# Kernel tuning notes

Hardware: AMD Instinct MI355X
Metric: run time of the kernel (lower is better)

Reference implementation:

```python
import jax, jax.numpy as jnp
import numpy as np
import math

E = 768      # embed_dim
N = 16       # ssm state_dim
K = 4        # d_conv
R = 48       # dt_rank = ceil(E/16)
DEPTH = 4
V = 32000    # vocab
B = 2
L = 1024
T = 100
H = 4 * E    # mlp hidden


def layer_norm(x, g, b):
    mu = jnp.mean(x, axis=-1, keepdims=True)
    var = jnp.mean(jnp.square(x - mu), axis=-1, keepdims=True)
    return (x - mu) * jax.lax.rsqrt(var + 1e-5) * g + b


def sin_emb(t, dim):
    half = dim // 2
    freqs = jnp.exp(-math.log(10000.0) * jnp.arange(half, dtype=jnp.float32) / half)
    args = t.astype(jnp.float32)[:, None] * freqs
    return jnp.concatenate([jnp.sin(args), jnp.cos(args)], axis=-1)


def ssm_forward(x, z_w, p_w, conv_w, dtp_w, dtp_b, A_log, Dp, out_w):
    # x: (B, L, E)
    z = x @ z_w.T
    params = x @ p_w.T                      # (B, L, R+2N)
    dt_un, _B_unused, Cp = jnp.split(params, [R, R + N], axis=-1)
    dt = jax.nn.softplus(dt_un @ dtp_w.T + dtp_b)   # (B, L, E)
    # depthwise causal conv (torch pads both sides d_conv-1 then trims -> left pad only)
    xc = jax.lax.conv_general_dilated(
        jnp.transpose(x, (0, 2, 1)), conv_w, (1,), [(K - 1, 0)],
        feature_group_count=E, dimension_numbers=('NCH', 'OIH', 'NCH'))
    u = jax.nn.silu(jnp.transpose(xc, (0, 2, 1)))   # (B, L, E)
    A = -jnp.exp(A_log)                              # (E, N)
    A_t = jnp.exp(dt[..., None] * A)                 # (B, L, E, N)
    B_t = jnp.where(jnp.abs(A) < 1e-5, dt[..., None], (A_t - 1.0) / (A + 1e-10))
    # recurrence exactly as source: h[0]=B[0]*u[0]; h[t]=A[t-1]*h[t-1]+B[t-1]*u[t-1]
    h0 = B_t[:, 0] * u[:, 0, :, None]                # (B, E, N)
    xs = (jnp.moveaxis(A_t[:, :-1], 1, 0),
          jnp.moveaxis(B_t[:, :-1], 1, 0),
          jnp.moveaxis(u[:, :-1], 1, 0))
    def step(h, inp):
        a, b, uu = inp
        h = a * h + b * uu[..., None]
        return h, h
    _, hs = jax.lax.scan(step, h0, xs)               # (L-1, B, E, N)
    h_all = jnp.concatenate([h0[None], hs], axis=0)  # (L, B, E, N)
    y = jnp.einsum('bln,lben->ble', Cp, h_all)
    y = y + u * Dp
    return (y * jax.nn.silu(z)) @ out_w.T


def setup_inputs() -> dict:
    key = jax.random.key(0)
    ks = list(jax.random.split(key, 32))
    it = iter(ks)
    def nrm(shape, fan_in):
        return jax.random.normal(next(it), shape, jnp.float32) * np.sqrt(2.0 / fan_in)
    d = {}
    d['tokens'] = jax.random.randint(next(it), (B, L), 0, V + 1)
    d['timesteps'] = jax.random.randint(next(it), (B,), 0, T)
    d['tok_emb'] = jax.random.normal(next(it), (V + 1, E), jnp.float32) * 0.02
    d['time_w1'] = nrm((H, E), E); d['time_b1'] = jnp.zeros((H,), jnp.float32)
    d['time_w2'] = nrm((E, H), H); d['time_b2'] = jnp.zeros((E,), jnp.float32)
    d['ln1_g'] = jnp.ones((DEPTH, E), jnp.float32); d['ln1_b'] = jnp.zeros((DEPTH, E), jnp.float32)
    d['z_w'] = nrm((DEPTH, E, E), E)
    d['p_w'] = nrm((DEPTH, R + 2 * N, E), E)
    d['conv_w'] = jax.random.normal(next(it), (DEPTH, E, 1, K), jnp.float32) * np.sqrt(1.0 / K)
    s = R ** -0.5 * 0.1
    d['dtp_w'] = jax.random.uniform(next(it), (DEPTH, E, R), jnp.float32, -s, s)
    d['dtp_b'] = jnp.full((DEPTH, E), math.log(math.expm1(0.001)), jnp.float32)
    d['A_log'] = jnp.tile(jnp.log(jnp.arange(1, N + 1, dtype=jnp.float32)), (DEPTH, E, 1))
    d['D_param'] = jnp.ones((DEPTH, E), jnp.float32)
    d['out_w'] = nrm((DEPTH, E, E), E)
    d['ln2_g'] = jnp.ones((DEPTH, E), jnp.float32); d['ln2_b'] = jnp.zeros((DEPTH, E), jnp.float32)
    d['mlp_w1'] = nrm((DEPTH, H, E), E); d['mlp_b1'] = jnp.zeros((DEPTH, H), jnp.float32)
    d['mlp_w2'] = nrm((DEPTH, E, H), H); d['mlp_b2'] = jnp.zeros((DEPTH, E), jnp.float32)
    d['lnout_g'] = jnp.ones((E,), jnp.float32); d['lnout_b'] = jnp.zeros((E,), jnp.float32)
    d['head_w'] = nrm((V, E), E); d['head_b'] = jnp.zeros((V,), jnp.float32)
    return d


def reference(tokens, timesteps, tok_emb, time_w1, time_b1, time_w2, time_b2,
              ln1_g, ln1_b, z_w, p_w, conv_w, dtp_w, dtp_b, A_log, D_param, out_w,
              ln2_g, ln2_b, mlp_w1, mlp_b1, mlp_w2, mlp_b2,
              lnout_g, lnout_b, head_w, head_b):
    temb = sin_emb(timesteps, E)
    temb = jax.nn.silu(temb @ time_w1.T + time_b1) @ time_w2.T + time_b2
    x = tok_emb[tokens] + temb[:, None, :]           # (B, L, E)
    for i in range(DEPTH):
        x = x + ssm_forward(layer_norm(x, ln1_g[i], ln1_b[i]),
                            z_w[i], p_w[i], conv_w[i], dtp_w[i], dtp_b[i],
                            A_log[i], D_param[i], out_w[i])
        h = layer_norm(x, ln2_g[i], ln2_b[i])
        h = jax.nn.gelu(h @ mlp_w1[i].T + mlp_b1[i], approximate=False) @ mlp_w2[i].T + mlp_b2[i]
        x = x + h
    x = layer_norm(x, lnout_g, lnout_b)
    return x @ head_w.T + head_b                     # (B, L, V)
```

## Files before the change

kernel.cpp:

```cpp
#include <hip/hip_runtime.h>
#include <math.h>

#define EE 768
#define NS 16
#define RR 48
#define NDEPTH 4
#define NB 2
#define NL 1024
#define NH 3072
#define NV 32000
#define M_ROWS (NB*NL)
#define NC 64
#define CL 16
#define ZPW 896
#define LOG2E 1.44269504088896f
#define LN2   0.69314718055995f

typedef __attribute__((ext_vector_type(8))) __bf16 bf16x8;
typedef __attribute__((ext_vector_type(4))) __bf16 bf16x4;
typedef __attribute__((ext_vector_type(4))) float f32x4;

__device__ __forceinline__ void gl_lds16(const __bf16* g, __bf16* l){
  __builtin_amdgcn_global_load_lds(
      (const __attribute__((address_space(1))) void*)g,
      (__attribute__((address_space(3))) void*)l, 16, 0, 0);
}

enum { BE_STORE=0, BE_BIAS=1, BE_RESID=2, BE_BIAS_RESID=3, BE_BIAS_GELU_B16=4,
       BE_STORE_ZP=5 };

template<int EPI, int BMT, int BNT>
__global__ __launch_bounds__(256) void gemm_bf16(const __bf16* __restrict__ A,
    const __bf16* __restrict__ W, const float* __restrict__ bias,
    void* __restrict__ Cv, float* __restrict__ dtf, int N, int K, int gx, int gy)
{
  const int nwg = gx*gy;
  const int orig = blockIdx.x;
  const int q = nwg >> 3, r = nwg & 7;
  const int xcd = orig & 7, bse = orig >> 3;
  int wg = (xcd < r ? xcd*(q+1) : r*(q+1) + (xcd-r)*q) + bse;
  const int GN = 16;
  const int per = gy*GN;
  const int g = wg / per;
  const int gstart = g*GN;
  const int gw0 = gx - gstart;
  const int gw = (GN < gw0) ? GN : gw0;
  const int local = wg - g*per;
  const int bx = gstart + local % gw;
  const int by = local / gw;

  constexpr int MFR = BMT/32;
  constexpr int NFR = BNT/32;
  __shared__ __bf16 As[BMT][64];
  __shared__ __bf16 Ws[BNT][64];
  const int bm = by*BMT, bn = bx*BNT;
  const int tid = threadIdx.x;
  const int w = tid>>6, lane = tid&63;
  const int wr = w>>1, wc = w&1;
  const int fr = lane&15, kg = lane>>4;
  const int sr8 = lane>>3;
  const int sg  = lane&7;
  const int ksrc = ((sg ^ sr8) & 7)*8;

  f32x4 acc[MFR][NFR];
  #pragma unroll
  for (int m=0;m<MFR;m++)
    #pragma unroll
    for (int n=0;n<NFR;n++)
      acc[m][n] = (f32x4){0.f,0.f,0.f,0.f};

  for (int k0=0;k0<K;k0+=64){
    const __bf16* gA = A + (size_t)(bm + w*(BMT/4) + sr8)*K + k0 + ksrc;
    #pragma unroll
    for (int c8=0;c8<BMT/32;c8++)
      gl_lds16(gA + (size_t)(c8*8)*K, &As[w*(BMT/4) + c8*8][0]);
    const __bf16* gW = W + (size_t)(bn + w*(BNT/4) + sr8)*K + k0 + ksrc;
    #pragma unroll
    for (int c8=0;c8<BNT/32;c8++)
      gl_lds16(gW + (size_t)(c8*8)*K, &Ws[w*(BNT/4) + c8*8][0]);
    __syncthreads();
    #pragma unroll
    for (int kk=0;kk<2;kk++){
      const int sp = (((kg + kk*4) ^ (fr&7)) & 7) * 8;
      bf16x8 af[MFR], bfr[NFR];
      #pragma unroll
      for (int m=0;m<MFR;m++) af[m]  = *(const bf16x8*)&As[wr*(BMT/2) + m*16 + fr][sp];
      #pragma unroll
      for (int n=0;n<NFR;n++) bfr[n] = *(const bf16x8*)&Ws[wc*(BNT/2) + n*16 + fr][sp];
      #pragma unroll
      for (int m=0;m<MFR;m++)
        #pragma unroll
        for (int n=0;n<NFR;n++)
          acc[m][n] = __builtin_amdgcn_mfma_f32_16x16x32_bf16(af[m], bfr[n], acc[m][n], 0,0,0);
    }
    __syncthreads();
  }

  float* Cf = (float*)Cv;
  __bf16* Cb = (__bf16*)Cv;
  #pragma unroll
  for (int m=0;m<MFR;m++){
    int row = bm + wr*(BMT/2) + m*16 + kg*4;
    #pragma unroll
    for (int n=0;n<NFR;n++){
      int col = bn + wc*(BNT/2) + n*16 + fr;
      float bsv = 0.f;
      if (EPI==BE_BIAS || EPI==BE_BIAS_RESID || EPI==BE_BIAS_GELU_B16)
        bsv = bias[col];
      #pragma unroll
      for (int rr2=0;rr2<4;rr2++){
        float v = acc[m][n][rr2];
        size_t idx = (size_t)(row+rr2)*N + col;
        if (EPI==BE_STORE)            Cf[idx] = v;
        else if (EPI==BE_BIAS)        Cf[idx] = v + bsv;
        else if (EPI==BE_RESID)       Cf[idx] += v;
        else if (EPI==BE_BIAS_RESID)  Cf[idx] += v + bsv;
        else if (EPI==BE_BIAS_GELU_B16){
          float xg = v + bsv; Cb[idx] = (__bf16)(0.5f*xg*(1.f+erff(xg*0.70710678118654752f)));
        } else if (EPI==BE_STORE_ZP){
          Cf[idx] = v;
          if (col >= 768 && col < 816) dtf[(size_t)(row+rr2)*RR + (col-768)] = v;
        }
      }
    }
  }
}

#define S1E 2752512LL
#define S2E 5111808LL
#define S3E 14548992LL
#define S4E 23986176LL
#define STOT 48562176LL

__global__ void f2b_all(const float* __restrict__ zw, const float* __restrict__ pw,
                        const float* __restrict__ ow, const float* __restrict__ m1,
                        const float* __restrict__ m2, const float* __restrict__ hw,
                        __bf16* __restrict__ o){
  long long idx = ((long long)blockIdx.x*256 + threadIdx.x)*4;
  if (idx >= STOT) return;
  float4 v;
  if (idx < S1E){
    long long layer = idx / (ZPW*EE);
    int rem = (int)(idx - layer*(ZPW*EE));
    int row = rem / EE, col = rem - (rem/EE)*EE;
    if (row < 768)      v = *(const float4*)(zw + ((size_t)layer*EE + row)*EE + col);
    else if (row < 848) v = *(const float4*)(pw + ((size_t)layer*80 + (row-768))*EE + col);
    else                v = make_float4(0.f,0.f,0.f,0.f);
  }
  else if (idx < S2E) v = *(const float4*)(ow + (idx - S1E));
  else if (idx < S3E) v = *(const float4*)(m1 + (idx - S2E));
  else if (idx < S4E) v = *(const float4*)(m2 + (idx - S3E));
  else                v = *(const float4*)(hw + (idx - S4E));
  bf16x4 rb = { (__bf16)v.x, (__bf16)v.y, (__bf16)v.z, (__bf16)v.w };
  *(bf16x4*)(o+idx) = rb;
}

__global__ __launch_bounds__(256) void ln_kernel(const float* __restrict__ x,
    const float* __restrict__ gp, const float* __restrict__ bp, __bf16* __restrict__ yb)
{
  int row = blockIdx.x;
  const float* xr = x + (size_t)row*EE;
  int t = threadIdx.x;
  float v0 = xr[t], v1 = xr[t+256], v2 = xr[t+512];
  float s = v0+v1+v2;
  #pragma unroll
  for (int m=1;m<64;m<<=1) s += __shfl_xor(s, m, 64);
  __shared__ float red[4], red2[4];
  int wid = t>>6;
  if ((t&63)==0) red[wid]=s;
  __syncthreads();
  float mu = (red[0]+red[1]+red[2]+red[3]) * (1.f/768.f);
  float d0=v0-mu, d1=v1-mu, d2=v2-mu;
  float qq = d0*d0+d1*d1+d2*d2;
  #pragma unroll
  for (int m=1;m<64;m<<=1) qq += __shfl_xor(qq, m, 64);
  if ((t&63)==0) red2[wid]=qq;
  __syncthreads();
  float var = (red2[0]+red2[1]+red2[2]+red2[3]) * (1.f/768.f);
  float inv = 1.0f/sqrtf(var + 1e-5f);
  __bf16* ybr = yb + (size_t)row*EE;
  ybr[t]     = (__bf16)(d0*inv*gp[t]     + bp[t]);
  ybr[t+256] = (__bf16)(d1*inv*gp[t+256] + bp[t+256]);
  ybr[t+512] = (__bf16)(d2*inv*gp[t+512] + bp[t+512]);
}

__global__ void sinemb_kernel(const int* __restrict__ timesteps, float* __restrict__ emb){
  int i = blockIdx.x*256+threadIdx.x;
  if (i >= NB*EE) return;
  int b = i/EE, e = i - b*EE;
  int half = EE/2;
  int j = (e<half)? e : e-half;
  float freq = expf(-logf(10000.f)*(float)j/(float)half);
  float arg = (float)timesteps[b]*freq;
  emb[i] = (e<half)? sinf(arg) : cosf(arg);
}

__global__ void time_mlp1(const float* __restrict__ emb, const float* __restrict__ w1,
                          const float* __restrict__ b1, float* __restrict__ thid){
  int wid = (blockIdx.x*256 + threadIdx.x)>>6;
  int lane = threadIdx.x & 63;
  int b = wid / NH, h = wid - b*NH;
  const float* er = emb + b*EE;
  const float* wr = w1 + (size_t)h*EE;
  float s = 0.f;
  #pragma unroll
  for (int j=0;j<EE/64;j++) s = fmaf(er[j*64+lane], wr[j*64+lane], s);
  #pragma unroll
  for (int m=1;m<64;m<<=1) s += __shfl_xor(s, m, 64);
  if (lane==0){
    s += b1[h];
    thid[wid] = s/(1.f+expf(-s));
  }
}

__global__ void time_mlp2(const float* __restrict__ thid, const float* __restrict__ w2,
                          const float* __restrict__ b2, float* __restrict__ temb){
  int wid = (blockIdx.x*256 + threadIdx.x)>>6;
  int lane = threadIdx.x & 63;
  int b = wid / EE, e = wid - b*EE;
  const float* tr = thid + b*NH;
  const float* wr = w2 + (size_t)e*NH;
  float s = 0.f;
  #pragma unroll
  for (int j=0;j<NH/64;j++) s = fmaf(tr[j*64+lane], wr[j*64+lane], s);
  #pragma unroll
  for (int m=1;m<64;m<<=1) s += __shfl_xor(s, m, 64);
  if (lane==0) temb[wid] = s + b2[e];
}

__global__ void embed_kernel(const int* __restrict__ tokens, const float* __restrict__ tok_emb,
                             const float* __restrict__ temb, float* __restrict__ x){
  int idx = blockIdx.x*256+threadIdx.x;
  int e = idx % EE; int bl = idx / EE; int b = bl / NL;
  int tok = tokens[bl];
  x[idx] = tok_emb[(size_t)tok*EE + e] + temb[b*EE + e];
}

__device__ __forceinline__ float dot48(const float* __restrict__ row, const float* wdf){
  float a0=0.f,a1=0.f,a2=0.f,a3=0.f;
  #pragma unroll
  for (int j=0;j<12;j++){
    float4 v = *(const float4*)(row + j*4);
    a0 = fmaf(v.x, wdf[j*4+0], a0);
    a1 = fmaf(v.y, wdf[j*4+1], a1);
    a2 = fmaf(v.z, wdf[j*4+2], a2);
    a3 = fmaf(v.w, wdf[j*4+3], a3);
  }
  return (a0+a1)+(a2+a3);
}
__device__ __forceinline__ float softplus_f(float x){
  return fmaxf(x,0.f) + LN2*log2f(1.f + exp2f(-LOG2E*fabsf(x)));
}
__device__ __forceinline__ float silu_f(float x){
  return x/(1.f + exp2f(-LOG2E*x));
}

__global__ __launch_bounds__(512) void scan_fused(
    const __bf16* __restrict__ xnb, const float* __restrict__ dtun,
    const float* __restrict__ dtw, const float* __restrict__ dtbias,
    const float* __restrict__ cwp, const float* __restrict__ A_log,
    const float* __restrict__ Dp, const float* __restrict__ zp,
    __bf16* __restrict__ gb)
{
  __shared__ float Pl[NC][8][NS];
  __shared__ float Sl[NC][8][NS];
  const int tid = threadIdx.x;
  const int e_l = tid & 7, c = tid >> 3;
  const int b  = blockIdx.x / (EE/8);
  const int eg = blockIdx.x % (EE/8);
  const int e  = eg*8 + e_l;

  float wdf[48];
  #pragma unroll
  for (int j=0;j<12;j++){
    float4 v = *(const float4*)(dtw + (size_t)e*RR + j*4);
    wdf[j*4]=v.x; wdf[j*4+1]=v.y; wdf[j*4+2]=v.z; wdf[j*4+3]=v.w;
  }
  float4 cw = *(const float4*)(cwp + e*4);
  float bias = dtbias[e];
  float Dv = Dp[e];
  float Av2[NS], iAv[NS];
  #pragma unroll
  for (int n4=0;n4<4;n4++){
    float4 v = *(const float4*)(A_log + (size_t)e*NS + n4*4);
    float a0=-exp2f(LOG2E*v.x), a1=-exp2f(LOG2E*v.y), a2=-exp2f(LOG2E*v.z), a3=-exp2f(LOG2E*v.w);
    Av2[n4*4+0]=a0*LOG2E; Av2[n4*4+1]=a1*LOG2E; Av2[n4*4+2]=a2*LOG2E; Av2[n4*4+3]=a3*LOG2E;
    iAv[n4*4+0]=1.f/(a0+1e-10f); iAv[n4*4+1]=1.f/(a1+1e-10f);
    iAv[n4*4+2]=1.f/(a2+1e-10f); iAv[n4*4+3]=1.f/(a3+1e-10f);
  }
  const __bf16* xcol = xnb + (size_t)b*NL*EE + e;
  const float* dtrow0 = dtun + (size_t)b*NL*RR;
  const int cs = c*CL;

  {
    float xw0,xw1,xw2,xw3;
    int prow = (c==0)? 0 : cs-1;
    xw0 = (prow-3>=0)? (float)xcol[(size_t)(prow-3)*EE] : 0.f;
    xw1 = (prow-2>=0)? (float)xcol[(size_t)(prow-2)*EE] : 0.f;
    xw2 = (prow-1>=0)? (float)xcol[(size_t)(prow-1)*EE] : 0.f;
    xw3 = (float)xcol[(size_t)prow*EE];
    float up  = silu_f(cw.x*xw0 + cw.y*xw1 + cw.z*xw2 + cw.w*xw3);
    float dtp_ = softplus_f(dot48(dtrow0 + (size_t)prow*RR, wdf) + bias);
    float h[NS];
    float sumdt = 0.f;
    #pragma unroll
    for (int n=0;n<NS;n++) h[n]=0.f;
    for (int i=0;i<CL;i++){
      int tt = cs+i;
      bool z0 = (tt==0);
      sumdt += dtp_;
      #pragma unroll
      for (int n=0;n<NS;n++){
        float at = exp2f(dtp_*Av2[n]);
        float bt = (at-1.f)*iAv[n];
        float s = bt*up;
        h[n] = z0 ? s : fmaf(at, h[n], s);
      }
      if (i<CL-1 && tt>0){
        xw0=xw1; xw1=xw2; xw2=xw3; xw3 = (float)xcol[(size_t)tt*EE];
        up  = silu_f(cw.x*xw0 + cw.y*xw1 + cw.z*xw2 + cw.w*xw3);
        dtp_ = softplus_f(dot48(dtrow0 + (size_t)tt*RR, wdf) + bias);
      }
    }
    #pragma unroll
    for (int n4=0;n4<4;n4++){
      float4 pv;
      if (c==0) pv = make_float4(0.f,0.f,0.f,0.f);
      else pv = make_float4(exp2f(Av2[n4*4+0]*sumdt), exp2f(Av2[n4*4+1]*sumdt),
                            exp2f(Av2[n4*4+2]*sumdt), exp2f(Av2[n4*4+3]*sumdt));
      *(float4*)&Pl[c][e_l][n4*4] = pv;
      *(float4*)&Sl[c][e_l][n4*4] = make_float4(h[n4*4],h[n4*4+1],h[n4*4+2],h[n4*4+3]);
    }
  }
  __syncthreads();
  if (tid < 128){
    int el2 = tid & 7, n = tid >> 3;
    float hh = 0.f;
    for (int cc=0; cc<NC; cc++){
      float pp = Pl[cc][el2][n], ss = Sl[cc][el2][n];
      Pl[cc][el2][n] = hh;
      hh = fmaf(pp, hh, ss);
    }
  }
  __syncthreads();
  {
    float h[NS];
    #pragma unroll
    for (int n4=0;n4<4;n4++){
      float4 v = *(const float4*)&Pl[c][e_l][n4*4];
      h[n4*4]=v.x; h[n4*4+1]=v.y; h[n4*4+2]=v.z; h[n4*4+3]=v.w;
    }
    float xw0,xw1,xw2,xw3;
    int prow = (c==0)? 0 : cs-1;
    xw0 = (prow-3>=0)? (float)xcol[(size_t)(prow-3)*EE] : 0.f;
    xw1 = (prow-2>=0)? (float)xcol[(size_t)(prow-2)*EE] : 0.f;
    xw2 = (prow-1>=0)? (float)xcol[(size_t)(prow-1)*EE] : 0.f;
    xw3 = (float)xcol[(size_t)prow*EE];
    float up  = silu_f(cw.x*xw0 + cw.y*xw1 + cw.z*xw2 + cw.w*xw3);
    float dtp_ = softplus_f(dot48(dtrow0 + (size_t)prow*RR, wdf) + bias);
    for (int i=0;i<CL;i++){
      int tt = cs+i;
      bool z0 = (tt==0);
      #pragma unroll
      for (int n=0;n<NS;n++){
        float at = exp2f(dtp_*Av2[n]);
        float bt = (at-1.f)*iAv[n];
        float s = bt*up;
        h[n] = z0 ? s : fmaf(at, h[n], s);
      }
      float ucur;
      if (tt==0){ ucur = up; }
      else {
        xw0=xw1; xw1=xw2; xw2=xw3; xw3 = (float)xcol[(size_t)tt*EE];
        ucur = silu_f(cw.x*xw0 + cw.y*xw1 + cw.z*xw2 + cw.w*xw3);
      }
      const float* zr = zp + (size_t)(b*NL+tt)*ZPW;
      float y = 0.f;
      #pragma unroll
      for (int n4=0;n4<4;n4++){
        float4 cv = *(const float4*)(zr + 832 + n4*4);
        y = fmaf(cv.x, h[n4*4], y);   y = fmaf(cv.y, h[n4*4+1], y);
        y = fmaf(cv.z, h[n4*4+2], y); y = fmaf(cv.w, h[n4*4+3], y);
      }
      float zv = zr[e];
      gb[(size_t)(b*NL+tt)*EE + e] = (__bf16)((y + ucur*Dv)*silu_f(zv));
      if (i<CL-1 && tt>0){
        dtp_ = softplus_f(dot48(dtrow0 + (size_t)tt*RR, wdf) + bias);
      }
      up = ucur;
    }
  }
}

extern "C" void kernel_launch(void* const* d_in, const int* in_sizes, int n_in,
                              void* d_out, int out_size, void* d_ws, size_t ws_size,
                              hipStream_t stream) {
  const int*   tokens    = (const int*)d_in[0];
  const int*   timesteps = (const int*)d_in[1];
  const float* tok_emb   = (const float*)d_in[2];
  const float* time_w1   = (const float*)d_in[3];
  const float* time_b1   = (const float*)d_in[4];
  const float* time_w2   = (const float*)d_in[5];
  const float* time_b2   = (const float*)d_in[6];
  const float* ln1_g     = (const float*)d_in[7];
  const float* ln1_b     = (const float*)d_in[8];
  const float* z_w       = (const float*)d_in[9];
  const float* p_w       = (const float*)d_in[10];
  const float* conv_w    = (const float*)d_in[11];
  const float* dtp_w     = (const float*)d_in[12];
  const float* dtp_b     = (const float*)d_in[13];
  const float* A_log     = (const float*)d_in[14];
  const float* D_param   = (const float*)d_in[15];
  const float* out_w     = (const float*)d_in[16];
  const float* ln2_g     = (const float*)d_in[17];
  const float* ln2_b     = (const float*)d_in[18];
  const float* mlp_w1    = (const float*)d_in[19];
  const float* mlp_b1    = (const float*)d_in[20];
  const float* mlp_w2    = (const float*)d_in[21];
  const float* mlp_b2    = (const float*)d_in[22];
  const float* lnout_g   = (const float*)d_in[23];
  const float* lnout_b   = (const float*)d_in[24];
  const float* head_w    = (const float*)d_in[25];
  const float* head_b    = (const float*)d_in[26];
  float* out = (float*)d_out;

  float* ws = (float*)d_ws;
  float* x      = ws;
  float* zp     = x    + (size_t)M_ROWS*EE;
  float* dtun   = zp   + (size_t)M_ROWS*ZPW;
  float* emb    = dtun + (size_t)M_ROWS*RR;
  float* thid   = emb + NB*EE;
  __bf16* xnb   = (__bf16*)(thid + NB*NH);
  __bf16* gb    = xnb + (size_t)M_ROWS*EE;
  __bf16* hidb  = gb  + (size_t)M_ROWS*EE;
  __bf16* wzp   = hidb + (size_t)M_ROWS*NH;
  __bf16* wout  = wzp  + (size_t)NDEPTH*ZPW*EE;
  __bf16* wm1   = wout + (size_t)NDEPTH*EE*EE;
  __bf16* wm2   = wm1  + (size_t)NDEPTH*NH*EE;
  __bf16* whead = wm2  + (size_t)NDEPTH*EE*NH;

  f2b_all<<<(int)(STOT/4/256), 256, 0, stream>>>(z_w, p_w, out_w, mlp_w1, mlp_w2, head_w, wzp);

  sinemb_kernel<<<(NB*EE+255)/256, 256, 0, stream>>>(timesteps, emb);
  time_mlp1<<<NB*NH/4, 256, 0, stream>>>(emb, time_w1, time_b1, thid);
  time_mlp2<<<NB*EE/4, 256, 0, stream>>>(thid, time_w2, time_b2, emb);
  embed_kernel<<<M_ROWS*EE/256, 256, 0, stream>>>(tokens, tok_emb, emb, x);

  const int scan_grid = NB*EE/8;

  for (int i=0;i<NDEPTH;i++){
    const float* dtw = dtp_w + (size_t)i*EE*RR;
    const float* dtb = dtp_b + i*EE;
    const float* cwp = conv_w + (size_t)i*EE*4;
    const float* al  = A_log + (size_t)i*EE*NS;
    ln_kernel<<<M_ROWS, 256, 0, stream>>>(x, ln1_g + i*EE, ln1_b + i*EE, xnb);
    gemm_bf16<BE_STORE_ZP,64,64><<<14*32, 256, 0, stream>>>(
        xnb, wzp + (size_t)i*ZPW*EE, nullptr, zp, dtun, ZPW, EE, 14, 32);
    scan_fused<<<scan_grid, 512, 0, stream>>>(xnb, dtun, dtw, dtb, cwp, al,
        D_param + i*EE, zp, gb);
    gemm_bf16<BE_RESID,64,64><<<12*32, 256, 0, stream>>>(
        gb, wout + (size_t)i*EE*EE, nullptr, x, nullptr, EE, EE, 12, 32);
    ln_kernel<<<M_ROWS, 256, 0, stream>>>(x, ln2_g + i*EE, ln2_b + i*EE, xnb);
    gemm_bf16<BE_BIAS_GELU_B16,64,128><<<24*32, 256, 0, stream>>>(
        xnb, wm1 + (size_t)i*NH*EE, mlp_b1 + i*NH, hidb, nullptr, NH, EE, 24, 32);
    gemm_bf16<BE_BIAS_RESID,64,64><<<12*32, 256, 0, stream>>>(
        hidb, wm2 + (size_t)i*EE*NH, mlp_b2 + i*EE, x, nullptr, EE, NH, 12, 32);
  }
  ln_kernel<<<M_ROWS, 256, 0, stream>>>(x, lnout_g, lnout_b, xnb);
  gemm_bf16<BE_BIAS,128,128><<<250*16, 256, 0, stream>>>(
      xnb, whead, head_b, out, nullptr, NV, EE, 250, 16);
}
```

Before: 905.8 us.

## Split z/C outputs into compact buffers and halve scan block width

The z/p projection GEMM now writes z as bf16 into its own buffer, dt_un to dtun, and the C coefficients into a compact 16-wide fp32 buffer, instead of a full 896-wide fp32 zp array. The scan kernel reads z and C from these smaller buffers, cutting global write and read traffic. The scan also moves from 8 to 4 channels per block with 256 threads, doubling the grid to 384 blocks for better CU coverage. Rounding z to bf16 before the silu gate adds a small precision loss.

```diff
diff --git a/kernel.cpp b/kernel.cpp
--- a/kernel.cpp
+++ b/kernel.cpp
@@ -32,7 +32,8 @@
 template<int EPI, int BMT, int BNT>
 __global__ __launch_bounds__(256) void gemm_bf16(const __bf16* __restrict__ A,
     const __bf16* __restrict__ W, const float* __restrict__ bias,
-    void* __restrict__ Cv, float* __restrict__ dtf, int N, int K, int gx, int gy)
+    void* __restrict__ Cv, float* __restrict__ dtf, float* __restrict__ aux,
+    int N, int K, int gx, int gy)
 {
   const int nwg = gx*gy;
   const int orig = blockIdx.x;
@@ -118,8 +119,9 @@
         else if (EPI==BE_BIAS_GELU_B16){
           float xg = v + bsv; Cb[idx] = (__bf16)(0.5f*xg*(1.f+erff(xg*0.70710678118654752f)));
         } else if (EPI==BE_STORE_ZP){
-          Cf[idx] = v;
-          if (col >= 768 && col < 816) dtf[(size_t)(row+rr2)*RR + (col-768)] = v;
+          if (col < 768)                    Cb[(size_t)(row+rr2)*EE + col] = (__bf16)v;
+          else if (col < 816)               dtf[(size_t)(row+rr2)*RR + (col-768)] = v;
+          else if (col >= 832 && col < 848) aux[(size_t)(row+rr2)*16 + (col-832)] = v;
         }
       }
     }
@@ -255,20 +257,20 @@
   return x/(1.f + exp2f(-LOG2E*x));
 }
 
-__global__ __launch_bounds__(512) void scan_fused(
+__global__ __launch_bounds__(256) void scan_fused(
     const __bf16* __restrict__ xnb, const float* __restrict__ dtun,
     const float* __restrict__ dtw, const float* __restrict__ dtbias,
     const float* __restrict__ cwp, const float* __restrict__ A_log,
-    const float* __restrict__ Dp, const float* __restrict__ zp,
-    __bf16* __restrict__ gb)
+    const float* __restrict__ Dp, const float* __restrict__ cpf,
+    const __bf16* __restrict__ zgb, __bf16* __restrict__ gb)
 {
-  __shared__ float Pl[NC][8][NS];
-  __shared__ float Sl[NC][8][NS];
+  __shared__ float Pl[NC][4][NS];
+  __shared__ float Sl[NC][4][NS];
   const int tid = threadIdx.x;
-  const int e_l = tid & 7, c = tid >> 3;
-  const int b  = blockIdx.x / (EE/8);
-  const int eg = blockIdx.x % (EE/8);
-  const int e  = eg*8 + e_l;
+  const int e_l = tid & 3, c = tid >> 2;
+  const int b  = blockIdx.x / (EE/4);
+  const int eg = blockIdx.x % (EE/4);
+  const int e  = eg*4 + e_l;
 
   float wdf[48];
   #pragma unroll
@@ -333,8 +335,8 @@
     }
   }
   __syncthreads();
-  if (tid < 128){
-    int el2 = tid & 7, n = tid >> 3;
+  if (tid < 64){
+    int el2 = tid & 3, n = tid >> 2;
     float hh = 0.f;
     for (int cc=0; cc<NC; cc++){
       float pp = Pl[cc][el2][n], ss = Sl[cc][el2][n];
@@ -374,15 +376,15 @@
         xw0=xw1; xw1=xw2; xw2=xw3; xw3 = (float)xcol[(size_t)tt*EE];
         ucur = silu_f(cw.x*xw0 + cw.y*xw1 + cw.z*xw2 + cw.w*xw3);
       }
-      const float* zr = zp + (size_t)(b*NL+tt)*ZPW;
+      const float* cpr = cpf + (size_t)(b*NL+tt)*16;
       float y = 0.f;
       #pragma unroll
       for (int n4=0;n4<4;n4++){
-        float4 cv = *(const float4*)(zr + 832 + n4*4);
+        float4 cv = *(const float4*)(cpr + n4*4);
         y = fmaf(cv.x, h[n4*4], y);   y = fmaf(cv.y, h[n4*4+1], y);
         y = fmaf(cv.z, h[n4*4+2], y); y = fmaf(cv.w, h[n4*4+3], y);
       }
-      float zv = zr[e];
+      float zv = (float)zgb[(size_t)(b*NL+tt)*EE + e];
       gb[(size_t)(b*NL+tt)*EE + e] = (__bf16)((y + ucur*Dv)*silu_f(zv));
       if (i<CL-1 && tt>0){
         dtp_ = softplus_f(dot48(dtrow0 + (size_t)tt*RR, wdf) + bias);
@@ -426,12 +428,13 @@
 
   float* ws = (float*)d_ws;
   float* x      = ws;
-  float* zp     = x    + (size_t)M_ROWS*EE;
-  float* dtun   = zp   + (size_t)M_ROWS*ZPW;
+  float* cpf    = x    + (size_t)M_ROWS*EE;
+  float* dtun   = cpf  + (size_t)M_ROWS*16;
   float* emb    = dtun + (size_t)M_ROWS*RR;
   float* thid   = emb + NB*EE;
   __bf16* xnb   = (__bf16*)(thid + NB*NH);
-  __bf16* gb    = xnb + (size_t)M_ROWS*EE;
+  __bf16* zgb   = xnb + (size_t)M_ROWS*EE;
+  __bf16* gb    = zgb + (size_t)M_ROWS*EE;
   __bf16* hidb  = gb  + (size_t)M_ROWS*EE;
   __bf16* wzp   = hidb + (size_t)M_ROWS*NH;
   __bf16* wout  = wzp  + (size_t)NDEPTH*ZPW*EE;
@@ -446,7 +449,7 @@
   time_mlp2<<<NB*EE/4, 256, 0, stream>>>(thid, time_w2, time_b2, emb);
   embed_kernel<<<M_ROWS*EE/256, 256, 0, stream>>>(tokens, tok_emb, emb, x);
 
-  const int scan_grid = NB*EE/8;
+  const int scan_grid = NB*EE/4;
 
   for (int i=0;i<NDEPTH;i++){
     const float* dtw = dtp_w + (size_t)i*EE*RR;
@@ -455,18 +458,18 @@
     const float* al  = A_log + (size_t)i*EE*NS;
     ln_kernel<<<M_ROWS, 256, 0, stream>>>(x, ln1_g + i*EE, ln1_b + i*EE, xnb);
     gemm_bf16<BE_STORE_ZP,64,64><<<14*32, 256, 0, stream>>>(
-        xnb, wzp + (size_t)i*ZPW*EE, nullptr, zp, dtun, ZPW, EE, 14, 32);
-    scan_fused<<<scan_grid, 512, 0, stream>>>(xnb, dtun, dtw, dtb, cwp, al,
-        D_param + i*EE, zp, gb);
+        xnb, wzp + (size_t)i*ZPW*EE, nullptr, zgb, dtun, cpf, ZPW, EE, 14, 32);
+    scan_fused<<<scan_grid, 256, 0, stream>>>(xnb, dtun, dtw, dtb, cwp, al,
+        D_param + i*EE, cpf, zgb, gb);
     gemm_bf16<BE_RESID,64,64><<<12*32, 256, 0, stream>>>(
-        gb, wout + (size_t)i*EE*EE, nullptr, x, nullptr, EE, EE, 12, 32);
+        gb, wout + (size_t)i*EE*EE, nullptr, x, nullptr, nullptr, EE, EE, 12, 32);
     ln_kernel<<<M_ROWS, 256, 0, stream>>>(x, ln2_g + i*EE, ln2_b + i*EE, xnb);
     gemm_bf16<BE_BIAS_GELU_B16,64,128><<<24*32, 256, 0, stream>>>(
-        xnb, wm1 + (size_t)i*NH*EE, mlp_b1 + i*NH, hidb, nullptr, NH, EE, 24, 32);
+        xnb, wm1 + (size_t)i*NH*EE, mlp_b1 + i*NH, hidb, nullptr, nullptr, NH, EE, 24, 32);
     gemm_bf16<BE_BIAS_RESID,64,64><<<12*32, 256, 0, stream>>>(
-        hidb, wm2 + (size_t)i*EE*NH, mlp_b2 + i*EE, x, nullptr, EE, NH, 12, 32);
+        hidb, wm2 + (size_t)i*EE*NH, mlp_b2 + i*EE, x, nullptr, nullptr, EE, NH, 12, 32);
   }
   ln_kernel<<<M_ROWS, 256, 0, stream>>>(x, lnout_g, lnout_b, xnb);
   gemm_bf16<BE_BIAS,128,128><<<250*16, 256, 0, stream>>>(
-      xnb, whead, head_b, out, nullptr, NV, EE, 250, 16);
-}
+      xnb, whead, head_b, out, nullptr, nullptr, NV, EE, 250, 16);
+}
```

Measured after the change: 910.4 us. About the same (+0.5%).
